# Kernel optimization log

Measured on AMD Instinct MI355X. Metric: run time of the kernel, lower is better.

Reference implementation:

```python
import jax, jax.numpy as jnp
import numpy as np

N_HEADS = 16
D_EMBED = 1024
N_CROSS = 768
D_HEAD = D_EMBED // N_HEADS


def setup_inputs() -> dict:
    key = jax.random.key(0)
    ks = jax.random.split(key, 10)
    B, S = 2, 2048
    x = jax.random.normal(ks[0], (B, S, D_EMBED), dtype=jnp.float32)
    context = jax.random.normal(ks[1], (B, S, N_CROSS), dtype=jnp.float32)
    sq = 1.0 / np.sqrt(D_EMBED)
    sc = 1.0 / np.sqrt(N_CROSS)
    Wq = jax.random.normal(ks[2], (D_EMBED, D_EMBED), dtype=jnp.float32) * sq
    bq = jnp.zeros((D_EMBED,), dtype=jnp.float32)
    Wk = jax.random.normal(ks[3], (N_CROSS, D_EMBED), dtype=jnp.float32) * sc
    bk = jnp.zeros((D_EMBED,), dtype=jnp.float32)
    Wv = jax.random.normal(ks[4], (N_CROSS, D_EMBED), dtype=jnp.float32) * sc
    bv = jnp.zeros((D_EMBED,), dtype=jnp.float32)
    Wo = jax.random.normal(ks[5], (D_EMBED, D_EMBED), dtype=jnp.float32) * sq
    bo = jnp.zeros((D_EMBED,), dtype=jnp.float32)
    return {"x": x, "context": context, "Wq": Wq, "bq": bq, "Wk": Wk, "bk": bk,
            "Wv": Wv, "bv": bv, "Wo": Wo, "bo": bo}


def reference(x, context, Wq, bq, Wk, bk, Wv, bv, Wo, bo):
    B, S, _ = x.shape

    def split_heads(t):  # [B,S,E] -> [B,H,S,Dh]
        return t.reshape(B, S, N_HEADS, D_HEAD).transpose(0, 2, 1, 3)

    q = split_heads(x @ Wq + bq)
    k = split_heads(context @ Wk + bk)
    v = split_heads(context @ Wv + bv)

    scale = 1.0 / np.sqrt(D_HEAD)
    scores = jnp.einsum('bhqd,bhkd->bhqk', q, k) * scale
    attn = jax.nn.softmax(scores, axis=-1)
    out = jnp.einsum('bhqk,bhkd->bhqd', attn, v)
    out = out.transpose(0, 2, 1, 3).reshape(B, S, D_EMBED)
    return out @ Wo + bo
```

## Files before the change

### kernel.cpp

```cpp
#include <hip/hip_runtime.h>
#include <math.h>


namespace {

typedef short bfr __attribute__((ext_vector_type(8)));
typedef short s4v __attribute__((ext_vector_type(4)));
typedef unsigned u4v __attribute__((ext_vector_type(4)));
typedef float accf __attribute__((ext_vector_type(16)));

#define MFMA32(a, b, c) __builtin_amdgcn_mfma_f32_32x32x16_bf16(a, b, c, 0, 0, 0)

__device__ inline short f2bf(float f) {
    unsigned u = __float_as_uint(f);
    u += 0x7fffu + ((u >> 16) & 1u);
    return (short)(u >> 16);
}
__device__ inline float bf2f(short s) {
    return __uint_as_float(((unsigned)(unsigned short)s) << 16);
}
__device__ inline float fexp2(float x) { return __builtin_amdgcn_exp2f(x); }
__device__ inline accf zero16() {
    accf z;
#pragma unroll
    for (int i = 0; i < 16; ++i) z[i] = 0.f;
    return z;
}
__device__ inline void dma16(const void* g, void* l) {
    __builtin_amdgcn_global_load_lds(
        (const __attribute__((address_space(1))) void*)g,
        (__attribute__((address_space(3))) void*)l, 16, 0, 0);
}

__global__ __launch_bounds__(256) void prep(
    const float* __restrict__ x, const float* __restrict__ ctx,
    short* __restrict__ xb, short* __restrict__ cb,
    const float* __restrict__ Wq, const float* __restrict__ Wk,
    const float* __restrict__ Wv, const float* __restrict__ Wo,
    short* __restrict__ Wqt, short* __restrict__ Wkt,
    short* __restrict__ Wvt, short* __restrict__ Wot) {
    __shared__ short t[64][68];
    const int bx = blockIdx.x;
    if (bx < 7168) {
        int i = bx * 256 + threadIdx.x;
        if (i < 1048576) {
            float4 v = ((const float4*)x)[i];
            s4v p = {f2bf(v.x), f2bf(v.y), f2bf(v.z), f2bf(v.w)};
            ((s4v*)xb)[i] = p;
        } else {
            int j = i - 1048576;
            float4 v = ((const float4*)ctx)[j];
            s4v p = {f2bf(v.x), f2bf(v.y), f2bf(v.z), f2bf(v.w)};
            ((s4v*)cb)[j] = p;
        }
        return;
    }
    const int idx = bx - 7168;
    const int z = idx >> 8, gy = (idx >> 4) & 15, gx = idx & 15;
    const float* W;
    short* Wt;
    int K;
    switch (z) {
        case 0: W = Wq; Wt = Wqt; K = 1024; break;
        case 1: W = Wk; Wt = Wkt; K = 768; break;
        case 2: W = Wv; Wt = Wvt; K = 768; break;
        default: W = Wo; Wt = Wot; K = 1024; break;
    }
    const int k0 = gy * 64;
    if (k0 >= K) return;
    const int tid = threadIdx.x;
    const int n0 = gx * 64;
    const int kr = tid >> 4, nc = (tid & 15) * 4;
#pragma unroll
    for (int rep = 0; rep < 4; ++rep) {
        int k = kr + rep * 16;
        float4 v = *(const float4*)&W[(size_t)(k0 + k) * 1024 + n0 + nc];
        t[nc + 0][k] = f2bf(v.x);
        t[nc + 1][k] = f2bf(v.y);
        t[nc + 2][k] = f2bf(v.z);
        t[nc + 3][k] = f2bf(v.w);
    }
    __syncthreads();
    const int nr = tid >> 4, kc = (tid & 15) * 4;
#pragma unroll
    for (int rep = 0; rep < 4; ++rep) {
        int n = nr + rep * 16;
        s4v p = {t[n][kc], t[n][kc + 1], t[n][kc + 2], t[n][kc + 3]};
        *(s4v*)&Wt[(size_t)(n0 + n) * K + k0 + kc] = p;
    }
}

__global__ __launch_bounds__(512, 6) void gemm_qkv(
    const short* __restrict__ xb, const short* __restrict__ cb,
    const short* __restrict__ Wqt, const short* __restrict__ Wkt,
    const short* __restrict__ Wvt, const float* __restrict__ bq,
    const float* __restrict__ bk, const float* __restrict__ bv,
    short* __restrict__ Qf, short* __restrict__ Kf, short* __restrict__ Vt,
    float qscale) {
    const int bid = blockIdx.x;
    const int z = bid >> 8;
    const int local = bid & 255;
    const short* A  = (z == 0) ? xb : cb;
    const short* Bt = (z == 0) ? Wqt : ((z == 1) ? Wkt : Wvt);
    const float* bias = (z == 0) ? bq : ((z == 1) ? bk : bv);
    const int K = (z == 0) ? 1024 : 768;
    const int NIT = K / 32;
    const float scale = (z == 0) ? qscale : 1.f;
    short* out = (z == 0) ? Qf : ((z == 1) ? Kf : Vt);

    __shared__ short As[8192];
    __shared__ short Bs[8192];
    const int t = threadIdx.x, lane = t & 63, w = t >> 6;
    const int lm = lane & 31, h2 = lane >> 5;
    const int wm = w & 1, wn = w >> 1;
    const int m0 = (local & 31) * 128, n0 = (local >> 5) * 128;

    const int st = t ^ ((t >> 3) & 7);
    const int srow = st >> 2, scol = (st & 3) * 8;
    const short* ga = A + (size_t)(m0 + srow) * K + scol;
    const short* gb = Bt + (size_t)(n0 + srow) * K + scol;

    const int xorv = (lm >> 1) & 7;
    const int rA0 = wm * 64 + lm, rB0 = wn * 32 + lm;

    accf acc[2] = {zero16(), zero16()};

    dma16(ga, &As[w * 512]);
    dma16(gb, &Bs[w * 512]);

#pragma unroll 1
    for (int it = 0; it < NIT; ++it) {
        const int p = it & 1;
        __syncthreads();
        if (it + 1 < NIT) {
            const int kt = (it + 1) * 32;
            dma16(ga + kt, &As[(1 - p) * 4096 + w * 512]);
            dma16(gb + kt, &Bs[(1 - p) * 4096 + w * 512]);
        }
        const short* bA = &As[p * 4096];
        const short* bB = &Bs[p * 4096];
#pragma unroll
        for (int kk8 = 0; kk8 < 4; kk8 += 2) {
            bfr a0 = *(const bfr*)&bA[((rA0 * 4 + h2 + kk8) ^ xorv) * 8];
            bfr a1 = *(const bfr*)&bA[(((rA0 + 32) * 4 + h2 + kk8) ^ xorv) * 8];
            bfr b0 = *(const bfr*)&bB[((rB0 * 4 + h2 + kk8) ^ xorv) * 8];
            acc[0] = MFMA32(a0, b0, acc[0]);
            acc[1] = MFMA32(a1, b0, acc[1]);
        }
    }

    const int n = n0 + wn * 32 + lm;
    const float bn = bias[n];
    const int hh = n >> 6, dd = n & 63;
#pragma unroll
    for (int mt = 0; mt < 2; ++mt) {
        const int mbase = m0 + wm * 64 + mt * 32 + 4 * h2;
        if (z != 2) {
            const int cb2 = (dd >> 4) * 512 + ((dd >> 3) & 1) * 256 + (dd & 7);
#pragma unroll
            for (int r = 0; r < 16; ++r) {
                const int m = mbase + (r & 3) + 8 * (r >> 2);
                const int bb = m >> 11, q = m & 2047;
                float v = (acc[mt][r] + bn) * scale;
                out[((size_t)((bb * 16 + hh) * 64 + (q >> 5))) * 2048 +
                    cb2 + (q & 31) * 8] = f2bf(v);
            }
        } else {
            const int dblk = dd >> 5, lmv = dd & 31;
#pragma unroll
            for (int g = 0; g < 4; ++g) {
                const int m = mbase + 8 * g;
                const int bb = m >> 11, s = m & 2047;
                const int kvt = s >> 6, kc = (s >> 4) & 3;
                const int h2v = (s >> 3) & 1, j0 = s & 7;
                s4v pq = {f2bf(acc[mt][4 * g + 0] + bn),
                          f2bf(acc[mt][4 * g + 1] + bn),
                          f2bf(acc[mt][4 * g + 2] + bn),
                          f2bf(acc[mt][4 * g + 3] + bn)};
                *(s4v*)(out +
                        ((size_t)(((bb * 16 + hh) * 32 + kvt) * 2 + dblk)) * 2048 +
                        kc * 512 + h2v * 256 + lmv * 8 + j0) = pq;
            }
        }
    }
}

__global__ __launch_bounds__(512) void gemm_out(
    const short* __restrict__ p0, const short* __restrict__ p1,
    const float* __restrict__ lsum, const short* __restrict__ Bt,
    const float* __restrict__ bias, float* __restrict__ out) {
    constexpr int K = 1024, NIT = 32;
    __shared__ short As[8192];
    __shared__ short Bs[8192];
    const int t = threadIdx.x, lane = t & 63, w = t >> 6;
    const int lm = lane & 31, h2 = lane >> 5;
    const int wm = w & 1, wn = w >> 1;
    const int bid = blockIdx.x;
    const int m0 = (bid & 31) * 128, n0 = (bid >> 5) * 128;

    const int st = t ^ ((t >> 3) & 7);
    const int srow = st >> 2, scol = (st & 3) * 8;
    const int gm = m0 + srow;
    const int b = gm >> 11, q = gm & 2047;
    const short* pa0 = p0 + (size_t)gm * 1024 + scol;
    const short* pa1 = p1 + (size_t)gm * 1024 + scol;
    const short* gb = Bt + (size_t)(n0 + srow) * K + scol;

    float inv[16];
#pragma unroll
    for (int h = 0; h < 16; ++h) {
        float l0 = lsum[((size_t)b * 16 + h) * 2048 + q];
        float l1 = lsum[((size_t)(2 + b) * 16 + h) * 2048 + q];
        inv[h] = 1.f / (l0 + l1);
    }

    const int xorv = (lm >> 1) & 7;
    const int rA0 = wm * 64 + lm, rB0 = wn * 32 + lm;

    accf acc[2] = {zero16(), zero16()};

    dma16(gb, &Bs[w * 512]);
    {
        bfr v0 = *(const bfr*)pa0;
        bfr v1 = *(const bfr*)pa1;
        const float iv = inv[0];
        bfr pk;
#pragma unroll
        for (int j = 0; j < 8; ++j)
            pk[j] = f2bf((bf2f(v0[j]) + bf2f(v1[j])) * iv);
        *(bfr*)&As[t * 8] = pk;
    }

#pragma unroll 1
    for (int it = 0; it < NIT; ++it) {
        const int p = it & 1;
        __syncthreads();
        bfr v0, v1;
        const bool nxt = (it + 1 < NIT);
        if (nxt) {
            const int ktn = (it + 1) * 32;
            dma16(gb + ktn, &Bs[(1 - p) * 4096 + w * 512]);
            v0 = *(const bfr*)(pa0 + ktn);
            v1 = *(const bfr*)(pa1 + ktn);
        }
        const short* bA = &As[p * 4096];
        const short* bB = &Bs[p * 4096];
#pragma unroll
        for (int kk8 = 0; kk8 < 4; kk8 += 2) {
            bfr a0 = *(const bfr*)&bA[((rA0 * 4 + h2 + kk8) ^ xorv) * 8];
            bfr a1 = *(const bfr*)&bA[(((rA0 + 32) * 4 + h2 + kk8) ^ xorv) * 8];
            bfr b0 = *(const bfr*)&bB[((rB0 * 4 + h2 + kk8) ^ xorv) * 8];
            acc[0] = MFMA32(a0, b0, acc[0]);
            acc[1] = MFMA32(a1, b0, acc[1]);
        }
        if (nxt) {
            const float iv = inv[(it + 1) >> 1];
            bfr pk;
#pragma unroll
            for (int j = 0; j < 8; ++j)
                pk[j] = f2bf((bf2f(v0[j]) + bf2f(v1[j])) * iv);
            *(bfr*)&As[(1 - p) * 4096 + t * 8] = pk;
        }
    }

    const int n = n0 + wn * 32 + lm;
    const float bn = bias[n];
#pragma unroll
    for (int mt = 0; mt < 2; ++mt) {
        const int mbase = m0 + wm * 64 + mt * 32 + 4 * h2;
#pragma unroll
        for (int r = 0; r < 16; ++r) {
            const int m = mbase + (r & 3) + 8 * (r >> 2);
            out[(size_t)m * 1024 + n] = acc[mt][r] + bn;
        }
    }
}

__global__ __launch_bounds__(256, 3) void attn(
    const short* __restrict__ Qf, const short* __restrict__ Kf,
    const short* __restrict__ Vt, short* __restrict__ part,
    float* __restrict__ lsum, int qhalf) {
    __shared__ short smem[16384];
    const int bid = blockIdx.x;
    const int hidx = bid & 31, qs = bid >> 5;
    const int split = qs & 1, qb = (qs >> 1) + qhalf * 8;
    const int b = hidx >> 4, h = hidx & 15;
    const int lane = threadIdx.x & 63, wv = threadIdx.x >> 6;
    const int lm = lane & 31, h2 = lane >> 5;
    const bool hb = h2 != 0;
    const int q0 = qb * 128 + wv * 32;

    const short* qbase =
        Qf + ((size_t)(hidx * 64 + (q0 >> 5))) * 2048 + lane * 8;
    bfr qf[4];
#pragma unroll
    for (int kc = 0; kc < 4; ++kc) qf[kc] = *(const bfr*)(qbase + kc * 512);

    const short* khead = Kf + (size_t)hidx * 131072 + split * 65536;
    const short* vhead = Vt + (size_t)hidx * 131072 + split * 65536;
    const short* gsrc =
        ((wv < 2) ? (khead + wv * 2048) : (vhead + (wv - 2) * 2048)) + lane * 8;

#pragma unroll
    for (int i = 0; i < 4; ++i)
        dma16(gsrc + i * 512, &smem[wv * 2048 + i * 512]);

    accf oa0 = zero16(), oa1 = zero16();
    float la0 = 0.f, la1 = 0.f;

#pragma unroll 1
    for (int it = 0; it < 16; ++it) {
        const int p = it & 1;
        __syncthreads();
        if (it + 1 < 16) {
            const short* gn = gsrc + (size_t)(it + 1) * 4096;
            short* ln = &smem[(1 - p) * 8192 + wv * 2048];
#pragma unroll
            for (int i = 0; i < 4; ++i) dma16(gn + i * 512, ln + i * 512);
        }
        const short* kb = &smem[p * 8192];
        bfr kf0[4], kf1[4], vf0[4], vf1[4];
#pragma unroll
        for (int kc = 0; kc < 4; ++kc) {
            kf0[kc] = *(const bfr*)&kb[kc * 512 + lane * 8];
            kf1[kc] = *(const bfr*)&kb[2048 + kc * 512 + lane * 8];
            vf0[kc] = *(const bfr*)&kb[4096 + kc * 512 + lane * 8];
            vf1[kc] = *(const bfr*)&kb[6144 + kc * 512 + lane * 8];
        }
        accf s0 = zero16(), s1 = zero16();
#pragma unroll
        for (int kc = 0; kc < 4; ++kc) {
            s0 = MFMA32(kf0[kc], qf[kc], s0);
            s1 = MFMA32(kf1[kc], qf[kc], s1);
        }

#pragma unroll
        for (int i = 0; i < 16; ++i) s0[i] = fexp2(s0[i]);
#pragma unroll
        for (int i = 0; i < 16; ++i) s1[i] = fexp2(s1[i]);
#pragma unroll
        for (int i = 0; i < 16; ++i) {
            if (i & 1) la1 += s0[i] + s1[i];
            else       la0 += s0[i] + s1[i];
        }

        bfr pb[4];
#pragma unroll
        for (int kc = 0; kc < 4; ++kc) {
            const accf& s = (kc < 2) ? s0 : s1;
            const int base = 8 * (kc & 1);
            unsigned Lw0 = __builtin_amdgcn_perm(__float_as_uint(s[base + 1]),
                                                 __float_as_uint(s[base + 0]),
                                                 0x07060302u);
            unsigned Lw1 = __builtin_amdgcn_perm(__float_as_uint(s[base + 3]),
                                                 __float_as_uint(s[base + 2]),
                                                 0x07060302u);
            unsigned Hw0 = __builtin_amdgcn_perm(__float_as_uint(s[base + 5]),
                                                 __float_as_uint(s[base + 4]),
                                                 0x07060302u);
            unsigned Hw1 = __builtin_amdgcn_perm(__float_as_uint(s[base + 7]),
                                                 __float_as_uint(s[base + 6]),
                                                 0x07060302u);
            unsigned c0 = hb ? Lw0 : Hw0;
            unsigned c1 = hb ? Lw1 : Hw1;
            unsigned r0 = (unsigned)__shfl_xor((int)c0, 32);
            unsigned r1 = (unsigned)__shfl_xor((int)c1, 32);
            u4v pw = {hb ? r0 : Lw0, hb ? r1 : Lw1,
                      hb ? Hw0 : r0, hb ? Hw1 : r1};
            pb[kc] = __builtin_bit_cast(bfr, pw);
        }

#pragma unroll
        for (int kc = 0; kc < 4; ++kc) {
            oa0 = MFMA32(vf0[kc], pb[kc], oa0);
            oa1 = MFMA32(vf1[kc], pb[kc], oa1);
        }
    }

    float ls = la0 + la1;
    ls += __shfl_xor(ls, 32);
    if (!hb) lsum[((size_t)(split * 2 + b) * 16 + h) * 2048 + q0 + lm] = ls;

    short* orow = part + (size_t)split * 4194304 +
                  (size_t)(b * 2048 + q0 + lm) * 1024 + h * 64;
#pragma unroll
    for (int dt = 0; dt < 2; ++dt) {
        const accf& oa = dt ? oa1 : oa0;
#pragma unroll
        for (int g = 0; g < 4; ++g) {
            const int d0 = dt * 32 + 4 * h2 + 8 * g;
            s4v p = {f2bf(oa[4 * g + 0]), f2bf(oa[4 * g + 1]),
                     f2bf(oa[4 * g + 2]), f2bf(oa[4 * g + 3])};
            *(s4v*)(orow + d0) = p;
        }
    }
}

}

extern "C" void kernel_launch(void* const* d_in, const int* in_sizes, int n_in,
                              void* d_out, int out_size, void* d_ws,
                              size_t ws_size, hipStream_t stream) {
    const float* x   = (const float*)d_in[0];
    const float* ctx = (const float*)d_in[1];
    const float* Wq  = (const float*)d_in[2];
    const float* bq  = (const float*)d_in[3];
    const float* Wk  = (const float*)d_in[4];
    const float* bk  = (const float*)d_in[5];
    const float* Wv  = (const float*)d_in[6];
    const float* bv  = (const float*)d_in[7];
    const float* Wo  = (const float*)d_in[8];
    const float* bo  = (const float*)d_in[9];

    short* xb  = (short*)d_ws;
    short* cb  = xb + (size_t)4096 * 1024;
    short* Wqt = cb + (size_t)4096 * 768;
    short* Wkt = Wqt + (size_t)1024 * 1024;
    short* Wvt = Wkt + (size_t)1024 * 768;
    short* Wot = Wvt + (size_t)1024 * 768;
    short* Qf  = Wot + (size_t)1024 * 1024;
    short* Kf  = Qf + (size_t)4096 * 1024;
    short* Vt  = Kf + (size_t)4096 * 1024;
    short* p0  = Vt + (size_t)4096 * 1024;
    short* p1  = p0 + (size_t)4096 * 1024;
    float* lsum = (float*)(p1 + (size_t)4096 * 1024);

    prep<<<8192, 256, 0, stream>>>(x, ctx, xb, cb, Wq, Wk, Wv, Wo,
                                   Wqt, Wkt, Wvt, Wot);

    const float qscale = 0.125f * 1.44269504088896f;
    gemm_qkv<<<768, 512, 0, stream>>>(xb, cb, Wqt, Wkt, Wvt,
                                      bq, bk, bv, Qf, Kf, Vt, qscale);

    attn<<<512, 256, 0, stream>>>(Qf, Kf, Vt, p0, lsum, 0);
    attn<<<512, 256, 0, stream>>>(Qf, Kf, Vt, p0, lsum, 1);

    gemm_out<<<256, 512, 0, stream>>>(p0, p1, lsum, Wot, bo, (float*)d_out);
}
```

Measured before the change: 215.1 us.

## Triple-buffer QKV GEMM loads with explicit vmcnt waits and merge attention launches

The QKV projection GEMM moves from double to triple buffering in shared memory. Two tiles are prefetched ahead, and the wait is an explicit s_waitcnt vmcnt(2) plus s_barrier in place of __syncthreads, so global loads can overlap further with the MFMA work. The two half-query attention launches become a single 1024-block launch, which removes one launch and the tail gap between them. The cost is more LDS per block, which may lower occupancy, and some redundant wrap-around loads on the last iterations.

```diff
diff --git a/kernel.cpp b/kernel.cpp
--- a/kernel.cpp
+++ b/kernel.cpp
@@ -108,8 +108,8 @@
     const float scale = (z == 0) ? qscale : 1.f;
     short* out = (z == 0) ? Qf : ((z == 1) ? Kf : Vt);
 
-    __shared__ short As[8192];
-    __shared__ short Bs[8192];
+    __shared__ short As[12288];
+    __shared__ short Bs[12288];
     const int t = threadIdx.x, lane = t & 63, w = t >> 6;
     const int lm = lane & 31, h2 = lane >> 5;
     const int wm = w & 1, wn = w >> 1;
@@ -127,18 +127,26 @@
 
     dma16(ga, &As[w * 512]);
     dma16(gb, &Bs[w * 512]);
-
+    __builtin_amdgcn_sched_barrier(0);
+    dma16(ga + 32, &As[4096 + w * 512]);
+    dma16(gb + 32, &Bs[4096 + w * 512]);
+    __builtin_amdgcn_sched_barrier(0);
+
+    int buf = 0;
 #pragma unroll 1
     for (int it = 0; it < NIT; ++it) {
-        const int p = it & 1;
-        __syncthreads();
-        if (it + 1 < NIT) {
-            const int kt = (it + 1) * 32;
-            dma16(ga + kt, &As[(1 - p) * 4096 + w * 512]);
-            dma16(gb + kt, &Bs[(1 - p) * 4096 + w * 512]);
-        }
-        const short* bA = &As[p * 4096];
-        const short* bB = &Bs[p * 4096];
+        __builtin_amdgcn_sched_barrier(0);
+        asm volatile("s_waitcnt vmcnt(2)" ::: "memory");
+        __builtin_amdgcn_s_barrier();
+        __builtin_amdgcn_sched_barrier(0);
+        {
+            const int nx = (it + 2 >= NIT) ? (it + 2 - NIT) : (it + 2);
+            const int nb = (buf + 2 >= 3) ? (buf - 1) : (buf + 2);
+            dma16(ga + nx * 32, &As[nb * 4096 + w * 512]);
+            dma16(gb + nx * 32, &Bs[nb * 4096 + w * 512]);
+        }
+        const short* bA = &As[buf * 4096];
+        const short* bB = &Bs[buf * 4096];
 #pragma unroll
         for (int kk8 = 0; kk8 < 4; kk8 += 2) {
             bfr a0 = *(const bfr*)&bA[((rA0 * 4 + h2 + kk8) ^ xorv) * 8];
@@ -147,7 +155,10 @@
             acc[0] = MFMA32(a0, b0, acc[0]);
             acc[1] = MFMA32(a1, b0, acc[1]);
         }
-    }
+        buf = (buf + 1 == 3) ? 0 : buf + 1;
+    }
+    asm volatile("s_waitcnt vmcnt(0)" ::: "memory");
+    __builtin_amdgcn_sched_barrier(0);
 
     const int n = n0 + wn * 32 + lm;
     const float bn = bias[n];
@@ -279,11 +290,11 @@
 __global__ __launch_bounds__(256, 3) void attn(
     const short* __restrict__ Qf, const short* __restrict__ Kf,
     const short* __restrict__ Vt, short* __restrict__ part,
-    float* __restrict__ lsum, int qhalf) {
+    float* __restrict__ lsum) {
     __shared__ short smem[16384];
     const int bid = blockIdx.x;
     const int hidx = bid & 31, qs = bid >> 5;
-    const int split = qs & 1, qb = (qs >> 1) + qhalf * 8;
+    const int split = qs & 1, qb = qs >> 1;
     const int b = hidx >> 4, h = hidx & 15;
     const int lane = threadIdx.x & 63, wv = threadIdx.x >> 6;
     const int lm = lane & 31, h2 = lane >> 5;
@@ -432,8 +443,7 @@
     gemm_qkv<<<768, 512, 0, stream>>>(xb, cb, Wqt, Wkt, Wvt,
                                       bq, bk, bv, Qf, Kf, Vt, qscale);
 
-    attn<<<512, 256, 0, stream>>>(Qf, Kf, Vt, p0, lsum, 0);
-    attn<<<512, 256, 0, stream>>>(Qf, Kf, Vt, p0, lsum, 1);
+    attn<<<1024, 256, 0, stream>>>(Qf, Kf, Vt, p0, lsum);
 
     gemm_out<<<256, 512, 0, stream>>>(p0, p1, lsum, Wot, bo, (float*)d_out);
 }
```

Result: faster. 208.2 us (-3.2%).
